# Kernel tuning notes

Measured on AMD Instinct MI355X. Metric: run time of the kernel, lower is better.

Reference implementation:

```python
import jax, jax.numpy as jnp
import numpy as np

# Static problem constants (must match setup_inputs)
NUM_GRAPHS = 64      # batch_size = int(batch[-1]) + 1
PTS_PER_GRAPH = 512
RATIO = 16           # centroids per graph
HEADS = 4
IN_CH = 64           # = out_channels per head (concat=False -> mean over heads)
NEG_SLOPE = 0.2


def setup_inputs() -> dict:
    key = jax.random.key(0)
    ks = jax.random.split(key, 8)
    N = NUM_GRAPHS * PTS_PER_GRAPH
    x = jax.random.normal(ks[0], (N, IN_CH), dtype=jnp.float32)
    edge_index = jnp.zeros((2, 2), dtype=jnp.int64)  # unused by forward
    batch = (jnp.arange(N) // PTS_PER_GRAPH).astype(jnp.int64)
    xcent_base = jax.random.normal(ks[1], (RATIO, IN_CH), dtype=jnp.float32)
    W_l = jax.random.normal(ks[2], (IN_CH, HEADS * IN_CH), dtype=jnp.float32) / np.sqrt(IN_CH)
    b_l = jax.random.normal(ks[3], (HEADS * IN_CH,), dtype=jnp.float32) * 0.01
    W_r = jax.random.normal(ks[4], (IN_CH, HEADS * IN_CH), dtype=jnp.float32) / np.sqrt(IN_CH)
    b_r = jax.random.normal(ks[5], (HEADS * IN_CH,), dtype=jnp.float32) * 0.01
    att = jax.random.normal(ks[6], (HEADS, IN_CH), dtype=jnp.float32) / np.sqrt(IN_CH)
    bias = jax.random.normal(ks[7], (IN_CH,), dtype=jnp.float32) * 0.01
    return {"x": x, "edge_index": edge_index, "batch": batch,
            "xcent_base": xcent_base, "W_l": W_l, "b_l": b_l,
            "W_r": W_r, "b_r": b_r, "att": att, "bias": bias}


def _bipart_pool(x, batch, xcent_base, W_l, b_l, W_r, b_r, att, bias):
    N = x.shape[0]
    B = NUM_GRAPHS
    Nc = B * RATIO  # number of centroid (target) nodes

    # Dense bipartite edges: each source node -> all RATIO centroids of its graph.
    src = jnp.repeat(jnp.arange(N, dtype=jnp.int32), RATIO)                     # [E]
    dst = jnp.tile(jnp.arange(RATIO, dtype=jnp.int32), N) \
        + jnp.repeat(batch.astype(jnp.int32), RATIO) * RATIO                    # [E]

    # PyG GATv2Conv(add_self_loops=True): remove src==dst edges, then add
    # self loops (i,i) for i < min(N_src, N_dst) = Nc. Keep static shapes by
    # masking the removed edges instead of deleting them.
    self_idx = jnp.arange(Nc, dtype=jnp.int32)
    src_f = jnp.concatenate([src, self_idx])
    dst_f = jnp.concatenate([dst, self_idx])
    drop = jnp.concatenate([src == dst, jnp.zeros((Nc,), dtype=bool)])          # [E+Nc]

    # Linear projections (source and target sides)
    x_l = (x @ W_l + b_l).reshape(N, HEADS, IN_CH)                              # [N,H,C]
    xcent = jnp.tile(xcent_base, (B, 1))                                        # [Nc,IN]
    x_r = (xcent @ W_r + b_r).reshape(Nc, HEADS, IN_CH)                         # [Nc,H,C]

    # GATv2 attention: leaky_relu(x_i + x_j) . att, softmax per target node
    xj = x_l[src_f]                                                             # [E',H,C]
    g = jax.nn.leaky_relu(xj + x_r[dst_f], NEG_SLOPE)
    alpha = jnp.einsum('ehc,hc->eh', g, att)                                    # [E',H]
    alpha = jnp.where(drop[:, None], jnp.float32(-1e30), alpha)
    amax = jax.ops.segment_max(alpha, dst_f, num_segments=Nc)                   # [Nc,H]
    e = jnp.exp(alpha - amax[dst_f])
    den = jax.ops.segment_sum(e, dst_f, num_segments=Nc)                        # [Nc,H]
    w = e / den[dst_f]                                                          # [E',H]

    out = jax.ops.segment_sum(w[..., None] * xj, dst_f, num_segments=Nc)        # [Nc,H,C]
    out = out.mean(axis=1) + bias                                               # concat=False -> mean heads
    return out.reshape(B, RATIO, IN_CH)


def reference(x, edge_index, batch, xcent_base, W_l, b_l, W_r, b_r, att, bias):
    xcent = _bipart_pool(x, batch, xcent_base, W_l, b_l, W_r, b_r, att, bias)
    batchcent = jnp.repeat(jnp.arange(NUM_GRAPHS, dtype=jnp.int64), RATIO)
    return xcent, batchcent
```

## Files before the change

### kernel.cpp

```cpp
#include <hip/hip_runtime.h>

#define PTS 512
#define CH  64

using s8v = __attribute__((ext_vector_type(8))) short;
using f4v = __attribute__((ext_vector_type(4))) float;

static __device__ __forceinline__ unsigned short f2b(float f) {
    unsigned u = __float_as_uint(f);
    return (unsigned short)((u + 0x7FFFu + ((u >> 16) & 1u)) >> 16);
}
static __device__ __forceinline__ float b2f(unsigned short s) {
    return __uint_as_float((unsigned)s << 16);
}

__global__ __launch_bounds__(256) void k0(
    const float* __restrict__ xcb, const float* __restrict__ W_r,
    const float* __restrict__ b_r, const float* __restrict__ att,
    const float* __restrict__ bias,
    float* __restrict__ xr_ws, float* __restrict__ sxr_ws,
    float* __restrict__ out)
{
    __shared__ float s_row[256];
    const int blk = blockIdx.x, tid = threadIdx.x;
    if (blk < 16) {
        const int h = blk >> 2, rq = blk & 3;
        const int rl = tid >> 6, c = tid & 63;
        const int r = rq * 4 + rl;
        float acc = b_r[h * 64 + c];
        for (int k = 0; k < 64; ++k)
            acc = fmaf(xcb[r * 64 + k], W_r[k * 256 + h * 64 + c], acc);
        xr_ws[(h * 16 + r) * 64 + c] = acc;
        s_row[rl * 64 + c] = acc;
        __syncthreads();
        if (tid < 4) {
            float s = 0.f;
            for (int cc = 0; cc < 64; ++cc)
                s = fmaf(s_row[tid * 64 + cc], att[h * 64 + cc], s);
            sxr_ws[h * 16 + rq * 4 + tid] = s;
        }
    } else if (blk < 32) {
        const int base = (blk - 16) * 4096;
        float4 bv = *(const float4*)(bias + ((tid * 4) & 63));
#pragma unroll
        for (int j = 0; j < 4; ++j)
            *(float4*)(out + base + j * 1024 + tid * 4) = bv;
    } else {
        const int c = tid * 4;
        *(float4*)(out + 65536 + c) = make_float4(
            (float)(c >> 4), (float)((c + 1) >> 4),
            (float)((c + 2) >> 4), (float)((c + 3) >> 4));
    }
}

__global__ __launch_bounds__(512, 1) void kmain(
    const float* __restrict__ x, const float* __restrict__ W_l,
    const float* __restrict__ b_l, const float* __restrict__ att,
    const float* __restrict__ xr_ws, const float* __restrict__ sxr_ws,
    float* __restrict__ out)
{
    __shared__ __align__(16) float s_buf[16384];
    __shared__ __align__(16) float s_e[8192];
    __shared__ __align__(16) unsigned short s_wt[4096];
    __shared__ __align__(16) float s_xls[1024];
    __shared__ __align__(16) float s_y[1024];
    __shared__ float s_dpart[128];
    __shared__ float s_es[16], s_dns[16], s_inv[16];

    unsigned short* s_xl   = (unsigned short*)s_buf;
    float*          s_part = s_buf;

    const int tid = threadIdx.x;
    const int h = blockIdx.x >> 6;
    const int b = blockIdx.x & 63;
    const int lane = tid & 63;
    const int w = __builtin_amdgcn_readfirstlane(tid >> 6);

    {
        const int c = tid >> 3, kk0 = (tid & 7) * 8;
        s8v wv;
#pragma unroll
        for (int j = 0; j < 8; ++j)
            wv[j] = (short)f2b(W_l[(kk0 + j) * 256 + h * 64 + c]);
        *(s8v*)&s_wt[c * 64 + (kk0 ^ ((c & 7) << 3))] = wv;
    }
    __syncthreads();

    {
        const int r0 = w * 2;
        const float* xg0 = x + (size_t)(b * 16 + r0) * 64;
        const float* xg1 = xg0 + 64;
        float a0 = b_l[h * 64 + lane], a1 = a0;
#pragma unroll
        for (int j8 = 0; j8 < 8; ++j8) {
            s8v wraw = *(const s8v*)&s_wt[lane * 64 + ((j8 * 8) ^ ((lane & 7) << 3))];
#pragma unroll
            for (int j = 0; j < 8; ++j) {
                const float wvf = b2f((unsigned short)wraw[j]);
                a0 = fmaf(xg0[j8 * 8 + j], wvf, a0);
                a1 = fmaf(xg1[j8 * 8 + j], wvf, a1);
            }
        }
        s_xls[r0 * 64 + lane] = a0;
        s_xls[(r0 + 1) * 64 + lane] = a1;

        const float at = att[h * 64 + lane];
        float sx0 = at * a0, ab0 = at * fabsf(a0 + xr_ws[(h * 16 + r0) * 64 + lane]);
        float sx1 = at * a1, ab1 = at * fabsf(a1 + xr_ws[(h * 16 + r0 + 1) * 64 + lane]);
#pragma unroll
        for (int off = 32; off >= 1; off >>= 1) {
            sx0 += __shfl_xor(sx0, off); ab0 += __shfl_xor(ab0, off);
            sx1 += __shfl_xor(sx1, off); ab1 += __shfl_xor(ab1, off);
        }
        if (lane == 0) {
            s_es[r0]     = __expf(0.6f * (sx0 + sxr_ws[h * 16 + r0])     + 0.4f * ab0);
            s_es[r0 + 1] = __expf(0.6f * (sx1 + sxr_ws[h * 16 + r0 + 1]) + 0.4f * ab1);
        }
    }

    {
        const int l15 = lane & 15, quad = lane >> 4;
        const size_t row0 = (size_t)b * PTS + w * 64;
        f4v acc[4][4];
        const f4v zf = {0.f, 0.f, 0.f, 0.f};
#pragma unroll
        for (int m = 0; m < 4; ++m)
#pragma unroll
            for (int n = 0; n < 4; ++n) acc[m][n] = zf;

#pragma unroll
        for (int ks = 0; ks < 2; ++ks) {
            s8v Af[4], Bf[4];
#pragma unroll
            for (int m = 0; m < 4; ++m) {
                const float* xp = x + (row0 + m * 16 + l15) * 64 + ks * 32 + quad * 8;
                float4 u0 = *(const float4*)xp;
                float4 u1 = *(const float4*)(xp + 4);
                s8v a;
                a[0] = (short)f2b(u0.x); a[1] = (short)f2b(u0.y);
                a[2] = (short)f2b(u0.z); a[3] = (short)f2b(u0.w);
                a[4] = (short)f2b(u1.x); a[5] = (short)f2b(u1.y);
                a[6] = (short)f2b(u1.z); a[7] = (short)f2b(u1.w);
                Af[m] = a;
            }
#pragma unroll
            for (int n = 0; n < 4; ++n) {
                const int cc = n * 16 + l15;
                Bf[n] = *(const s8v*)&s_wt[cc * 64 +
                        ((ks * 32 + quad * 8) ^ ((cc & 7) << 3))];
            }
#pragma unroll
            for (int m = 0; m < 4; ++m)
#pragma unroll
                for (int n = 0; n < 4; ++n)
                    acc[m][n] = __builtin_amdgcn_mfma_f32_16x16x32_bf16(
                        Af[m], Bf[n], acc[m][n], 0, 0, 0);
        }

        float blv[4];
#pragma unroll
        for (int n = 0; n < 4; ++n) blv[n] = b_l[h * 64 + n * 16 + l15];
#pragma unroll
        for (int m = 0; m < 4; ++m)
#pragma unroll
            for (int n = 0; n < 4; ++n) {
                const int cc = n * 16 + l15;
#pragma unroll
                for (int qq = 0; qq < 4; ++qq) {
                    const int row = w * 64 + m * 16 + quad * 4 + qq;
                    s_xl[row * 64 + (cc ^ ((row & 7) << 3))] =
                        f2b(acc[m][n][qq] + blv[n]);
                }
            }
    }
    __syncthreads();

    {
        const int i = tid, sw = i & 3, xsw = (i & 7) << 3;
        const float* attw = att + h * 64;
        const float* xrw  = xr_ws + h * 1024;
        float ac[16];
#pragma unroll
        for (int r = 0; r < 16; ++r) ac[r] = 0.f;
        float sxl = 0.f;

#pragma unroll
        for (int half = 0; half < 2; ++half) {
            const int cb = half * 32;
            float xlv[32], atv[32];
#pragma unroll
            for (int c8 = 0; c8 < 4; ++c8) {
                const int ch0 = cb + c8 * 8;
                uint4 raw = *(const uint4*)&s_xl[i * 64 + (ch0 ^ xsw)];
                unsigned uu[4] = {raw.x, raw.y, raw.z, raw.w};
#pragma unroll
                for (int p = 0; p < 4; ++p) {
                    xlv[c8 * 8 + 2 * p]     = __uint_as_float(uu[p] << 16);
                    xlv[c8 * 8 + 2 * p + 1] = __uint_as_float(uu[p] & 0xffff0000u);
                }
            }
#pragma unroll
            for (int cq = 0; cq < 8; ++cq) {
                float4 a4 = *(const float4*)(attw + cb + cq * 4);
                atv[cq * 4 + 0] = a4.x; atv[cq * 4 + 1] = a4.y;
                atv[cq * 4 + 2] = a4.z; atv[cq * 4 + 3] = a4.w;
            }
#pragma unroll
            for (int t = 0; t < 32; ++t) sxl = fmaf(atv[t], xlv[t], sxl);

#pragma unroll 2
            for (int r = 0; r < 16; ++r) {
                const float4* xrp = (const float4*)(xrw + r * 64 + cb);
                float a = 0.f;
#pragma unroll
                for (int cq = 0; cq < 8; ++cq) {
                    float4 x4 = xrp[cq];
                    a = fmaf(atv[cq * 4 + 0], fabsf(xlv[cq * 4 + 0] + x4.x), a);
                    a = fmaf(atv[cq * 4 + 1], fabsf(xlv[cq * 4 + 1] + x4.y), a);
                    a = fmaf(atv[cq * 4 + 2], fabsf(xlv[cq * 4 + 2] + x4.z), a);
                    a = fmaf(atv[cq * 4 + 3], fabsf(xlv[cq * 4 + 3] + x4.w), a);
                }
                ac[r] += a;
            }
        }
        float ev[16];
#pragma unroll
        for (int r = 0; r < 16; ++r) {
            float a = 0.6f * (sxl + sxr_ws[h * 16 + r]) + 0.4f * ac[r];
            float e = __expf(a);
            if (b == 0 && i == r) e = 0.f;
            ev[r] = e;
        }
        float4* se4 = (float4*)s_e;
#pragma unroll
        for (int q = 0; q < 4; ++q)
            se4[i * 4 + (q ^ sw)] = make_float4(ev[q * 4 + 0], ev[q * 4 + 1],
                                                ev[q * 4 + 2], ev[q * 4 + 3]);
#pragma unroll
        for (int r = 0; r < 16; ++r) {
            float s = ev[r];
#pragma unroll
            for (int off = 32; off >= 1; off >>= 1) s += __shfl_xor(s, off);
            if (lane == 0) s_dpart[w * 16 + r] = s;
        }
    }
    __syncthreads();

    if (tid < 16) {
        float dns = 0.f;
#pragma unroll
        for (int ww = 0; ww < 8; ++ww) dns += s_dpart[ww * 16 + tid];
        const float es = s_es[tid];
        s_dns[tid] = dns;
        s_inv[tid] = 1.f / (dns + es);
    }

    {
        const int kt = tid & 15, rt = (tid >> 4) & 3, is = tid >> 6;
        float y4[4][4];
#pragma unroll
        for (int i = 0; i < 4; ++i)
#pragma unroll
            for (int j = 0; j < 4; ++j) y4[i][j] = 0.f;

        const float* xb = x + ((size_t)b * PTS + is * 64) * 64;
        const float4* se4 = (const float4*)s_e;
        for (int ii0 = 0; ii0 < 64; ii0 += 8) {
            float4 xv[8], evv[8];
#pragma unroll
            for (int u = 0; u < 8; ++u)
                xv[u] = *(const float4*)(xb + (ii0 + u) * 64 + kt * 4);
#pragma unroll
            for (int u = 0; u < 8; ++u) {
                const int i = is * 64 + ii0 + u;
                evv[u] = se4[i * 4 + (rt ^ (i & 3))];
            }
#pragma unroll
            for (int u = 0; u < 8; ++u) {
                const float4 xvu = xv[u], ev = evv[u];
                y4[0][0] = fmaf(ev.x, xvu.x, y4[0][0]); y4[0][1] = fmaf(ev.x, xvu.y, y4[0][1]);
                y4[0][2] = fmaf(ev.x, xvu.z, y4[0][2]); y4[0][3] = fmaf(ev.x, xvu.w, y4[0][3]);
                y4[1][0] = fmaf(ev.y, xvu.x, y4[1][0]); y4[1][1] = fmaf(ev.y, xvu.y, y4[1][1]);
                y4[1][2] = fmaf(ev.y, xvu.z, y4[1][2]); y4[1][3] = fmaf(ev.y, xvu.w, y4[1][3]);
                y4[2][0] = fmaf(ev.z, xvu.x, y4[2][0]); y4[2][1] = fmaf(ev.z, xvu.y, y4[2][1]);
                y4[2][2] = fmaf(ev.z, xvu.z, y4[2][2]); y4[2][3] = fmaf(ev.z, xvu.w, y4[2][3]);
                y4[3][0] = fmaf(ev.w, xvu.x, y4[3][0]); y4[3][1] = fmaf(ev.w, xvu.y, y4[3][1]);
                y4[3][2] = fmaf(ev.w, xvu.z, y4[3][2]); y4[3][3] = fmaf(ev.w, xvu.w, y4[3][3]);
            }
        }
#pragma unroll
        for (int rr = 0; rr < 4; ++rr)
            *(float4*)&s_part[is * 1024 + (rt * 4 + rr) * 64 + kt * 4] =
                make_float4(y4[rr][0], y4[rr][1], y4[rr][2], y4[rr][3]);
    }
    __syncthreads();

    for (int o = tid; o < 1024; o += 512) {
        float s = 0.f;
#pragma unroll
        for (int sl = 0; sl < 8; ++sl) s += s_part[sl * 1024 + o];
        s_y[o] = s;
    }
    __syncthreads();

    for (int o = tid; o < 1024; o += 512) {
        const int r = o >> 6, ch = o & 63;
        float a = 0.f;
        const float* yr = s_y + r * 64;
#pragma unroll
        for (int k = 0; k < 64; ++k)
            a = fmaf(yr[k], W_l[k * 256 + h * 64 + ch], a);
        float val = (a + s_dns[r] * b_l[h * 64 + ch]
                     + s_es[r] * s_xls[r * 64 + ch]) * s_inv[r];
        atomicAdd(&out[(b * 16 + r) * 64 + ch], 0.25f * val);
    }
}

extern "C" void kernel_launch(void* const* d_in, const int* in_sizes, int n_in,
                              void* d_out, int out_size, void* d_ws, size_t ws_size,
                              hipStream_t stream) {
    (void)in_sizes; (void)n_in; (void)out_size; (void)ws_size;
    const float* x    = (const float*)d_in[0];
    const float* xcb  = (const float*)d_in[3];
    const float* W_l  = (const float*)d_in[4];
    const float* b_l  = (const float*)d_in[5];
    const float* W_r  = (const float*)d_in[6];
    const float* b_r  = (const float*)d_in[7];
    const float* att  = (const float*)d_in[8];
    const float* bias = (const float*)d_in[9];
    float* out = (float*)d_out;

    float* wsf = (float*)d_ws;
    float* xr_ws  = wsf;
    float* sxr_ws = wsf + 4096;

    hipLaunchKernelGGL(k0, dim3(33), dim3(256), 0, stream,
                       xcb, W_r, b_r, att, bias, xr_ws, sxr_ws, out);
    hipLaunchKernelGGL(kmain, dim3(256), dim3(512), 0, stream,
                       x, W_l, b_l, att, xr_ws, sxr_ws, out);
}
```

Baseline: 111.5 us.

## Split per-graph-head work into halves and add a finalize kernel replacing atomics

```diff
diff --git a/kernel.cpp b/kernel.cpp
--- a/kernel.cpp
+++ b/kernel.cpp
@@ -17,110 +17,68 @@
 __global__ __launch_bounds__(256) void k0(
     const float* __restrict__ xcb, const float* __restrict__ W_r,
     const float* __restrict__ b_r, const float* __restrict__ att,
-    const float* __restrict__ bias,
-    float* __restrict__ xr_ws, float* __restrict__ sxr_ws,
-    float* __restrict__ out)
+    float* __restrict__ xr_ws, float* __restrict__ sxr_ws)
 {
     __shared__ float s_row[256];
     const int blk = blockIdx.x, tid = threadIdx.x;
-    if (blk < 16) {
-        const int h = blk >> 2, rq = blk & 3;
-        const int rl = tid >> 6, c = tid & 63;
-        const int r = rq * 4 + rl;
-        float acc = b_r[h * 64 + c];
-        for (int k = 0; k < 64; ++k)
-            acc = fmaf(xcb[r * 64 + k], W_r[k * 256 + h * 64 + c], acc);
-        xr_ws[(h * 16 + r) * 64 + c] = acc;
-        s_row[rl * 64 + c] = acc;
-        __syncthreads();
-        if (tid < 4) {
-            float s = 0.f;
-            for (int cc = 0; cc < 64; ++cc)
-                s = fmaf(s_row[tid * 64 + cc], att[h * 64 + cc], s);
-            sxr_ws[h * 16 + rq * 4 + tid] = s;
-        }
-    } else if (blk < 32) {
-        const int base = (blk - 16) * 4096;
-        float4 bv = *(const float4*)(bias + ((tid * 4) & 63));
-#pragma unroll
-        for (int j = 0; j < 4; ++j)
-            *(float4*)(out + base + j * 1024 + tid * 4) = bv;
-    } else {
-        const int c = tid * 4;
-        *(float4*)(out + 65536 + c) = make_float4(
-            (float)(c >> 4), (float)((c + 1) >> 4),
-            (float)((c + 2) >> 4), (float)((c + 3) >> 4));
-    }
-}
-
-__global__ __launch_bounds__(512, 1) void kmain(
+    const int h = blk >> 2, rq = blk & 3;
+    const int rl = tid >> 6, c = tid & 63;
+    const int r = rq * 4 + rl;
+    float acc = b_r[h * 64 + c];
+    for (int k = 0; k < 64; ++k)
+        acc = fmaf(xcb[r * 64 + k], W_r[k * 256 + h * 64 + c], acc);
+    xr_ws[(h * 16 + r) * 64 + c] = acc;
+    s_row[rl * 64 + c] = acc;
+    __syncthreads();
+    if (tid < 4) {
+        float s = 0.f;
+        for (int cc = 0; cc < 64; ++cc)
+            s = fmaf(s_row[tid * 64 + cc], att[h * 64 + cc], s);
+        sxr_ws[h * 16 + rq * 4 + tid] = s;
+    }
+}
+
+__global__ __launch_bounds__(256, 2) void kmain(
     const float* __restrict__ x, const float* __restrict__ W_l,
     const float* __restrict__ b_l, const float* __restrict__ att,
     const float* __restrict__ xr_ws, const float* __restrict__ sxr_ws,
-    float* __restrict__ out)
+    float* __restrict__ y_ws, float* __restrict__ den_ws)
 {
-    __shared__ __align__(16) float s_buf[16384];
-    __shared__ __align__(16) float s_e[8192];
+    __shared__ __align__(16) float s_buf[8192];
+    __shared__ __align__(16) float s_e[4096];
     __shared__ __align__(16) unsigned short s_wt[4096];
-    __shared__ __align__(16) float s_xls[1024];
-    __shared__ __align__(16) float s_y[1024];
-    __shared__ float s_dpart[128];
-    __shared__ float s_es[16], s_dns[16], s_inv[16];
+    __shared__ float s_dpart[64];
 
     unsigned short* s_xl   = (unsigned short*)s_buf;
     float*          s_part = s_buf;
 
     const int tid = threadIdx.x;
-    const int h = blockIdx.x >> 6;
-    const int b = blockIdx.x & 63;
+    const int L = blockIdx.x;
+    const int j = L >> 3;
+    const int b = (L & 7) * 8 + (j >> 3);
+    const int h = (j & 7) >> 1;
+    const int half = j & 1;
+    const int bh2 = ((b * 4 + h) << 1) | half;
     const int lane = tid & 63;
     const int w = __builtin_amdgcn_readfirstlane(tid >> 6);
 
     {
-        const int c = tid >> 3, kk0 = (tid & 7) * 8;
-        s8v wv;
-#pragma unroll
-        for (int j = 0; j < 8; ++j)
-            wv[j] = (short)f2b(W_l[(kk0 + j) * 256 + h * 64 + c]);
-        *(s8v*)&s_wt[c * 64 + (kk0 ^ ((c & 7) << 3))] = wv;
-    }
-    __syncthreads();
-
-    {
-        const int r0 = w * 2;
-        const float* xg0 = x + (size_t)(b * 16 + r0) * 64;
-        const float* xg1 = xg0 + 64;
-        float a0 = b_l[h * 64 + lane], a1 = a0;
-#pragma unroll
-        for (int j8 = 0; j8 < 8; ++j8) {
-            s8v wraw = *(const s8v*)&s_wt[lane * 64 + ((j8 * 8) ^ ((lane & 7) << 3))];
-#pragma unroll
-            for (int j = 0; j < 8; ++j) {
-                const float wvf = b2f((unsigned short)wraw[j]);
-                a0 = fmaf(xg0[j8 * 8 + j], wvf, a0);
-                a1 = fmaf(xg1[j8 * 8 + j], wvf, a1);
-            }
-        }
-        s_xls[r0 * 64 + lane] = a0;
-        s_xls[(r0 + 1) * 64 + lane] = a1;
-
-        const float at = att[h * 64 + lane];
-        float sx0 = at * a0, ab0 = at * fabsf(a0 + xr_ws[(h * 16 + r0) * 64 + lane]);
-        float sx1 = at * a1, ab1 = at * fabsf(a1 + xr_ws[(h * 16 + r0 + 1) * 64 + lane]);
-#pragma unroll
-        for (int off = 32; off >= 1; off >>= 1) {
-            sx0 += __shfl_xor(sx0, off); ab0 += __shfl_xor(ab0, off);
-            sx1 += __shfl_xor(sx1, off); ab1 += __shfl_xor(ab1, off);
-        }
-        if (lane == 0) {
-            s_es[r0]     = __expf(0.6f * (sx0 + sxr_ws[h * 16 + r0])     + 0.4f * ab0);
-            s_es[r0 + 1] = __expf(0.6f * (sx1 + sxr_ws[h * 16 + r0 + 1]) + 0.4f * ab1);
-        }
-    }
+        const int c = tid >> 2, kq = tid & 3;
+#pragma unroll
+        for (int j8 = 0; j8 < 2; ++j8) {
+            const int kk = kq * 16 + j8 * 8;
+            s8v wv;
+#pragma unroll
+            for (int t = 0; t < 8; ++t)
+                wv[t] = (short)f2b(W_l[(kk + t) * 256 + h * 64 + c]);
+            *(s8v*)&s_wt[c * 64 + (kk ^ ((c & 7) << 3))] = wv;
+        }
+    }
+    __syncthreads();
 
     {
         const int l15 = lane & 15, quad = lane >> 4;
-        const size_t row0 = (size_t)b * PTS + w * 64;
+        const size_t row0 = (size_t)b * PTS + half * 256 + w * 64;
         f4v acc[4][4];
         const f4v zf = {0.f, 0.f, 0.f, 0.f};
 #pragma unroll
@@ -185,8 +143,8 @@
         float sxl = 0.f;
 
 #pragma unroll
-        for (int half = 0; half < 2; ++half) {
-            const int cb = half * 32;
+        for (int hf = 0; hf < 2; ++hf) {
+            const int cb = hf * 32;
             float xlv[32], atv[32];
 #pragma unroll
             for (int c8 = 0; c8 < 4; ++c8) {
@@ -228,7 +186,7 @@
         for (int r = 0; r < 16; ++r) {
             float a = 0.6f * (sxl + sxr_ws[h * 16 + r]) + 0.4f * ac[r];
             float e = __expf(a);
-            if (b == 0 && i == r) e = 0.f;
+            if (b == 0 && half == 0 && i == r) e = 0.f;
             ev[r] = e;
         }
         float4* se4 = (float4*)s_e;
@@ -247,12 +205,10 @@
     __syncthreads();
 
     if (tid < 16) {
-        float dns = 0.f;
-#pragma unroll
-        for (int ww = 0; ww < 8; ++ww) dns += s_dpart[ww * 16 + tid];
-        const float es = s_es[tid];
-        s_dns[tid] = dns;
-        s_inv[tid] = 1.f / (dns + es);
+        float d = 0.f;
+#pragma unroll
+        for (int ww = 0; ww < 4; ++ww) d += s_dpart[ww * 16 + tid];
+        den_ws[bh2 * 16 + tid] = d;
     }
 
     {
@@ -261,9 +217,9 @@
 #pragma unroll
         for (int i = 0; i < 4; ++i)
 #pragma unroll
-            for (int j = 0; j < 4; ++j) y4[i][j] = 0.f;
-
-        const float* xb = x + ((size_t)b * PTS + is * 64) * 64;
+            for (int jj = 0; jj < 4; ++jj) y4[i][jj] = 0.f;
+
+        const float* xb = x + ((size_t)b * PTS + half * 256 + is * 64) * 64;
         const float4* se4 = (const float4*)s_e;
         for (int ii0 = 0; ii0 < 64; ii0 += 8) {
             float4 xv[8], evv[8];
@@ -295,25 +251,96 @@
     }
     __syncthreads();
 
-    for (int o = tid; o < 1024; o += 512) {
+    for (int o = tid; o < 1024; o += 256) {
         float s = 0.f;
 #pragma unroll
-        for (int sl = 0; sl < 8; ++sl) s += s_part[sl * 1024 + o];
-        s_y[o] = s;
-    }
-    __syncthreads();
-
-    for (int o = tid; o < 1024; o += 512) {
-        const int r = o >> 6, ch = o & 63;
-        float a = 0.f;
-        const float* yr = s_y + r * 64;
-#pragma unroll
+        for (int sl = 0; sl < 4; ++sl) s += s_part[sl * 1024 + o];
+        y_ws[bh2 * 1024 + o] = s;
+    }
+}
+
+__global__ __launch_bounds__(256) void kfin(
+    const float* __restrict__ x, const float* __restrict__ W_l,
+    const float* __restrict__ b_l, const float* __restrict__ att,
+    const float* __restrict__ xr_ws, const float* __restrict__ sxr_ws,
+    const float* __restrict__ bias,
+    const float* __restrict__ y_ws, const float* __restrict__ den_ws,
+    float* __restrict__ out)
+{
+    __shared__ __align__(16) float s_yt[1024];
+    __shared__ __align__(16) float s_xls[1024];
+    __shared__ float s_dent[16], s_es[16];
+
+    const int tid = threadIdx.x;
+    const int b = blockIdx.x >> 2, rg = blockIdx.x & 3;
+
+#pragma unroll
+    for (int jj = 0; jj < 4; ++jj) {
+        const int flat = tid + jj * 256;
+        const int hh = flat >> 8, rl = (flat >> 6) & 3, k = flat & 63;
+        const size_t base = (size_t)((b * 4 + hh) * 2) * 1024 + (rg * 4 + rl) * 64 + k;
+        s_yt[flat] = y_ws[base] + y_ws[base + 1024];
+    }
+    if (tid < 16) {
+        const int hh = tid >> 2, rl = tid & 3;
+        const int base = ((b * 4 + hh) * 2) * 16 + rg * 4 + rl;
+        s_dent[tid] = den_ws[base] + den_ws[base + 16];
+    }
+#pragma unroll
+    for (int jj = 0; jj < 4; ++jj) {
+        const int flat = tid + jj * 256;
+        const int hh = flat >> 8, rl = (flat >> 6) & 3, c = flat & 63;
+        const int r = rg * 4 + rl;
+        float acc = b_l[hh * 64 + c];
         for (int k = 0; k < 64; ++k)
-            a = fmaf(yr[k], W_l[k * 256 + h * 64 + ch], a);
-        float val = (a + s_dns[r] * b_l[h * 64 + ch]
-                     + s_es[r] * s_xls[r * 64 + ch]) * s_inv[r];
-        atomicAdd(&out[(b * 16 + r) * 64 + ch], 0.25f * val);
-    }
+            acc = fmaf(x[(size_t)(b * 16 + r) * 64 + k],
+                       W_l[k * 256 + hh * 64 + c], acc);
+        s_xls[flat] = acc;
+    }
+    __syncthreads();
+
+    {
+        const int g = tid >> 4, l16 = tid & 15;
+        const int hh = g >> 2, rl = g & 3, r = rg * 4 + rl;
+        float sx = 0.f, ab = 0.f;
+#pragma unroll
+        for (int q = 0; q < 4; ++q) {
+            const int cc = l16 * 4 + q;
+            const float a = att[hh * 64 + cc];
+            const float xv = s_xls[(g << 6) + cc];
+            sx = fmaf(a, xv, sx);
+            ab = fmaf(a, fabsf(xv + xr_ws[(hh * 16 + r) * 64 + cc]), ab);
+        }
+#pragma unroll
+        for (int off = 8; off >= 1; off >>= 1) {
+            sx += __shfl_xor(sx, off);
+            ab += __shfl_xor(ab, off);
+        }
+        if (l16 == 0)
+            s_es[g] = __expf(0.6f * (sx + sxr_ws[hh * 16 + r]) + 0.4f * ab);
+    }
+    __syncthreads();
+
+    {
+        const int rl = tid >> 6, c = tid & 63;
+        const int r = rg * 4 + rl;
+        float num = 0.f;
+#pragma unroll
+        for (int hh = 0; hh < 4; ++hh) {
+            float t = 0.f;
+            const float* yr = s_yt + hh * 256 + rl * 64;
+#pragma unroll
+            for (int k = 0; k < 64; ++k)
+                t = fmaf(yr[k], W_l[k * 256 + hh * 64 + c], t);
+            const float es = s_es[hh * 4 + rl];
+            const float dt = s_dent[hh * 4 + rl];
+            num += (t + dt * b_l[hh * 64 + c] + es * s_xls[hh * 256 + rl * 64 + c])
+                   / (dt + es);
+        }
+        out[(size_t)(b * 16 + r) * 64 + c] = bias[c] + 0.25f * num;
+    }
+    if (rg == 0 && tid < 16)
+        out[65536 + b * 16 + tid] = (float)b;
 }
 
 extern "C" void kernel_launch(void* const* d_in, const int* in_sizes, int n_in,
@@ -333,9 +360,13 @@
     float* wsf = (float*)d_ws;
     float* xr_ws  = wsf;
     float* sxr_ws = wsf + 4096;
-
-    hipLaunchKernelGGL(k0, dim3(33), dim3(256), 0, stream,
-                       xcb, W_r, b_r, att, bias, xr_ws, sxr_ws, out);
-    hipLaunchKernelGGL(kmain, dim3(256), dim3(512), 0, stream,
-                       x, W_l, b_l, att, xr_ws, sxr_ws, out);
-}
+    float* y_ws   = wsf + 4224;
+    float* den_ws = wsf + 528512;
+
+    hipLaunchKernelGGL(k0, dim3(16), dim3(256), 0, stream,
+                       xcb, W_r, b_r, att, xr_ws, sxr_ws);
+    hipLaunchKernelGGL(kmain, dim3(512), dim3(256), 0, stream,
+                       x, W_l, b_l, att, xr_ws, sxr_ws, y_ws, den_ws);
+    hipLaunchKernelGGL(kfin, dim3(256), dim3(256), 0, stream,
+                       x, W_l, b_l, att, xr_ws, sxr_ws, bias, y_ws, den_ws, out);
+}
```

After: 123.6 us. 1.11x slower.

## Split each graph-head block into two point halves and reduce in a finalize kernel

Applied to the files above, without the earlier changes.

```diff
diff --git a/kernel.cpp b/kernel.cpp
--- a/kernel.cpp
+++ b/kernel.cpp
@@ -17,62 +17,49 @@
 __global__ __launch_bounds__(256) void k0(
     const float* __restrict__ xcb, const float* __restrict__ W_r,
     const float* __restrict__ b_r, const float* __restrict__ att,
-    const float* __restrict__ bias,
-    float* __restrict__ xr_ws, float* __restrict__ sxr_ws,
-    float* __restrict__ out)
+    float* __restrict__ xr_ws, float* __restrict__ sxr_ws)
 {
     __shared__ float s_row[256];
     const int blk = blockIdx.x, tid = threadIdx.x;
-    if (blk < 16) {
-        const int h = blk >> 2, rq = blk & 3;
-        const int rl = tid >> 6, c = tid & 63;
-        const int r = rq * 4 + rl;
-        float acc = b_r[h * 64 + c];
-        for (int k = 0; k < 64; ++k)
-            acc = fmaf(xcb[r * 64 + k], W_r[k * 256 + h * 64 + c], acc);
-        xr_ws[(h * 16 + r) * 64 + c] = acc;
-        s_row[rl * 64 + c] = acc;
-        __syncthreads();
-        if (tid < 4) {
-            float s = 0.f;
-            for (int cc = 0; cc < 64; ++cc)
-                s = fmaf(s_row[tid * 64 + cc], att[h * 64 + cc], s);
-            sxr_ws[h * 16 + rq * 4 + tid] = s;
-        }
-    } else if (blk < 32) {
-        const int base = (blk - 16) * 4096;
-        float4 bv = *(const float4*)(bias + ((tid * 4) & 63));
-#pragma unroll
-        for (int j = 0; j < 4; ++j)
-            *(float4*)(out + base + j * 1024 + tid * 4) = bv;
-    } else {
-        const int c = tid * 4;
-        *(float4*)(out + 65536 + c) = make_float4(
-            (float)(c >> 4), (float)((c + 1) >> 4),
-            (float)((c + 2) >> 4), (float)((c + 3) >> 4));
-    }
-}
-
-__global__ __launch_bounds__(512, 1) void kmain(
+    const int h = blk >> 2, rq = blk & 3;
+    const int rl = tid >> 6, c = tid & 63;
+    const int r = rq * 4 + rl;
+    float acc = b_r[h * 64 + c];
+    for (int k = 0; k < 64; ++k)
+        acc = fmaf(xcb[r * 64 + k], W_r[k * 256 + h * 64 + c], acc);
+    xr_ws[(h * 16 + r) * 64 + c] = acc;
+    s_row[rl * 64 + c] = acc;
+    __syncthreads();
+    if (tid < 4) {
+        float s = 0.f;
+        for (int cc = 0; cc < 64; ++cc)
+            s = fmaf(s_row[tid * 64 + cc], att[h * 64 + cc], s);
+        sxr_ws[h * 16 + rq * 4 + tid] = s;
+    }
+}
+
+__global__ __launch_bounds__(512, 4) void kmain(
     const float* __restrict__ x, const float* __restrict__ W_l,
     const float* __restrict__ b_l, const float* __restrict__ att,
     const float* __restrict__ xr_ws, const float* __restrict__ sxr_ws,
-    float* __restrict__ out)
+    float* __restrict__ num_ws, float* __restrict__ den_ws,
+    float* __restrict__ xls_ws, float* __restrict__ es_ws)
 {
-    __shared__ __align__(16) float s_buf[16384];
-    __shared__ __align__(16) float s_e[8192];
+    __shared__ __align__(16) float s_buf[8192];
+    __shared__ __align__(16) float s_e[4096];
     __shared__ __align__(16) unsigned short s_wt[4096];
-    __shared__ __align__(16) float s_xls[1024];
-    __shared__ __align__(16) float s_y[1024];
-    __shared__ float s_dpart[128];
-    __shared__ float s_es[16], s_dns[16], s_inv[16];
+    __shared__ float s_dpart[64];
 
     unsigned short* s_xl   = (unsigned short*)s_buf;
     float*          s_part = s_buf;
+    float*          s_y    = s_e;
 
     const int tid = threadIdx.x;
-    const int h = blockIdx.x >> 6;
-    const int b = blockIdx.x & 63;
+    const int b    = blockIdx.x >> 3;
+    const int h    = (blockIdx.x >> 1) & 3;
+    const int half = blockIdx.x & 1;
+    const int bh   = b * 4 + h;
+    const int bh2  = bh * 2 + half;
     const int lane = tid & 63;
     const int w = __builtin_amdgcn_readfirstlane(tid >> 6);
 
@@ -86,7 +73,7 @@
     }
     __syncthreads();
 
-    {
+    if (half == 0) {
         const int r0 = w * 2;
         const float* xg0 = x + (size_t)(b * 16 + r0) * 64;
         const float* xg1 = xg0 + 64;
@@ -101,8 +88,8 @@
                 a1 = fmaf(xg1[j8 * 8 + j], wvf, a1);
             }
         }
-        s_xls[r0 * 64 + lane] = a0;
-        s_xls[(r0 + 1) * 64 + lane] = a1;
+        xls_ws[bh * 1024 + r0 * 64 + lane]       = a0;
+        xls_ws[bh * 1024 + (r0 + 1) * 64 + lane] = a1;
 
         const float at = att[h * 64 + lane];
         float sx0 = at * a0, ab0 = at * fabsf(a0 + xr_ws[(h * 16 + r0) * 64 + lane]);
@@ -113,26 +100,28 @@
             sx1 += __shfl_xor(sx1, off); ab1 += __shfl_xor(ab1, off);
         }
         if (lane == 0) {
-            s_es[r0]     = __expf(0.6f * (sx0 + sxr_ws[h * 16 + r0])     + 0.4f * ab0);
-            s_es[r0 + 1] = __expf(0.6f * (sx1 + sxr_ws[h * 16 + r0 + 1]) + 0.4f * ab1);
+            es_ws[bh * 16 + r0] =
+                __expf(0.6f * (sx0 + sxr_ws[h * 16 + r0])     + 0.4f * ab0);
+            es_ws[bh * 16 + r0 + 1] =
+                __expf(0.6f * (sx1 + sxr_ws[h * 16 + r0 + 1]) + 0.4f * ab1);
         }
     }
 
     {
         const int l15 = lane & 15, quad = lane >> 4;
-        const size_t row0 = (size_t)b * PTS + w * 64;
-        f4v acc[4][4];
+        const size_t row0 = (size_t)b * PTS + half * 256 + w * 32;
+        f4v acc[2][4];
         const f4v zf = {0.f, 0.f, 0.f, 0.f};
 #pragma unroll
-        for (int m = 0; m < 4; ++m)
+        for (int m = 0; m < 2; ++m)
 #pragma unroll
             for (int n = 0; n < 4; ++n) acc[m][n] = zf;
 
 #pragma unroll
         for (int ks = 0; ks < 2; ++ks) {
-            s8v Af[4], Bf[4];
-#pragma unroll
-            for (int m = 0; m < 4; ++m) {
+            s8v Af[2], Bf[4];
+#pragma unroll
+            for (int m = 0; m < 2; ++m) {
                 const float* xp = x + (row0 + m * 16 + l15) * 64 + ks * 32 + quad * 8;
                 float4 u0 = *(const float4*)xp;
                 float4 u1 = *(const float4*)(xp + 4);
@@ -150,7 +139,7 @@
                         ((ks * 32 + quad * 8) ^ ((cc & 7) << 3))];
             }
 #pragma unroll
-            for (int m = 0; m < 4; ++m)
+            for (int m = 0; m < 2; ++m)
 #pragma unroll
                 for (int n = 0; n < 4; ++n)
                     acc[m][n] = __builtin_amdgcn_mfma_f32_16x16x32_bf16(
@@ -161,13 +150,13 @@
 #pragma unroll
         for (int n = 0; n < 4; ++n) blv[n] = b_l[h * 64 + n * 16 + l15];
 #pragma unroll
-        for (int m = 0; m < 4; ++m)
+        for (int m = 0; m < 2; ++m)
 #pragma unroll
             for (int n = 0; n < 4; ++n) {
                 const int cc = n * 16 + l15;
 #pragma unroll
                 for (int qq = 0; qq < 4; ++qq) {
-                    const int row = w * 64 + m * 16 + quad * 4 + qq;
+                    const int row = w * 32 + m * 16 + quad * 4 + qq;
                     s_xl[row * 64 + (cc ^ ((row & 7) << 3))] =
                         f2b(acc[m][n][qq] + blv[n]);
                 }
@@ -176,17 +165,18 @@
     __syncthreads();
 
     {
-        const int i = tid, sw = i & 3, xsw = (i & 7) << 3;
+        const int i = tid & 255, rh = tid >> 8, rbase = rh * 8;
+        const int sw = i & 3, xsw = (i & 7) << 3;
         const float* attw = att + h * 64;
         const float* xrw  = xr_ws + h * 1024;
-        float ac[16];
-#pragma unroll
-        for (int r = 0; r < 16; ++r) ac[r] = 0.f;
+        float ac[8];
+#pragma unroll
+        for (int r = 0; r < 8; ++r) ac[r] = 0.f;
         float sxl = 0.f;
 
 #pragma unroll
-        for (int half = 0; half < 2; ++half) {
-            const int cb = half * 32;
+        for (int hf = 0; hf < 2; ++hf) {
+            const int cb = hf * 32;
             float xlv[32], atv[32];
 #pragma unroll
             for (int c8 = 0; c8 < 4; ++c8) {
@@ -209,8 +199,8 @@
             for (int t = 0; t < 32; ++t) sxl = fmaf(atv[t], xlv[t], sxl);
 
 #pragma unroll 2
-            for (int r = 0; r < 16; ++r) {
-                const float4* xrp = (const float4*)(xrw + r * 64 + cb);
+            for (int rr = 0; rr < 8; ++rr) {
+                const float4* xrp = (const float4*)(xrw + (rbase + rr) * 64 + cb);
                 float a = 0.f;
 #pragma unroll
                 for (int cq = 0; cq < 8; ++cq) {
@@ -220,39 +210,38 @@
                     a = fmaf(atv[cq * 4 + 2], fabsf(xlv[cq * 4 + 2] + x4.z), a);
                     a = fmaf(atv[cq * 4 + 3], fabsf(xlv[cq * 4 + 3] + x4.w), a);
                 }
-                ac[r] += a;
-            }
-        }
-        float ev[16];
-#pragma unroll
-        for (int r = 0; r < 16; ++r) {
-            float a = 0.6f * (sxl + sxr_ws[h * 16 + r]) + 0.4f * ac[r];
+                ac[rr] += a;
+            }
+        }
+        float ev[8];
+#pragma unroll
+        for (int rr = 0; rr < 8; ++rr) {
+            const int r = rbase + rr;
+            float a = 0.6f * (sxl + sxr_ws[h * 16 + r]) + 0.4f * ac[rr];
             float e = __expf(a);
-            if (b == 0 && i == r) e = 0.f;
-            ev[r] = e;
+            if (b == 0 && half == 0 && i == r) e = 0.f;
+            ev[rr] = e;
         }
         float4* se4 = (float4*)s_e;
-#pragma unroll
-        for (int q = 0; q < 4; ++q)
-            se4[i * 4 + (q ^ sw)] = make_float4(ev[q * 4 + 0], ev[q * 4 + 1],
-                                                ev[q * 4 + 2], ev[q * 4 + 3]);
-#pragma unroll
-        for (int r = 0; r < 16; ++r) {
-            float s = ev[r];
+        se4[i * 4 + ((2 * rh)     ^ sw)] = make_float4(ev[0], ev[1], ev[2], ev[3]);
+        se4[i * 4 + ((2 * rh + 1) ^ sw)] = make_float4(ev[4], ev[5], ev[6], ev[7]);
+#pragma unroll
+        for (int rr = 0; rr < 8; ++rr) {
+            float s = ev[rr];
 #pragma unroll
             for (int off = 32; off >= 1; off >>= 1) s += __shfl_xor(s, off);
-            if (lane == 0) s_dpart[w * 16 + r] = s;
+            if (lane == 0) s_dpart[w * 8 + rr] = s;
         }
     }
     __syncthreads();
 
     if (tid < 16) {
-        float dns = 0.f;
-#pragma unroll
-        for (int ww = 0; ww < 8; ++ww) dns += s_dpart[ww * 16 + tid];
-        const float es = s_es[tid];
-        s_dns[tid] = dns;
-        s_inv[tid] = 1.f / (dns + es);
+        const int rh = tid >> 3;
+        float d = 0.f;
+#pragma unroll
+        for (int ww = 0; ww < 4; ++ww)
+            d += s_dpart[(rh * 4 + ww) * 8 + (tid & 7)];
+        den_ws[bh2 * 16 + tid] = d;
     }
 
     {
@@ -261,18 +250,18 @@
 #pragma unroll
         for (int i = 0; i < 4; ++i)
 #pragma unroll
-            for (int j = 0; j < 4; ++j) y4[i][j] = 0.f;
-
-        const float* xb = x + ((size_t)b * PTS + is * 64) * 64;
+            for (int jj = 0; jj < 4; ++jj) y4[i][jj] = 0.f;
+
+        const float* xb = x + ((size_t)b * PTS + half * 256 + is * 32) * 64;
         const float4* se4 = (const float4*)s_e;
-        for (int ii0 = 0; ii0 < 64; ii0 += 8) {
+        for (int ii0 = 0; ii0 < 32; ii0 += 8) {
             float4 xv[8], evv[8];
 #pragma unroll
             for (int u = 0; u < 8; ++u)
                 xv[u] = *(const float4*)(xb + (ii0 + u) * 64 + kt * 4);
 #pragma unroll
             for (int u = 0; u < 8; ++u) {
-                const int i = is * 64 + ii0 + u;
+                const int i = is * 32 + ii0 + u;
                 evv[u] = se4[i * 4 + (rt ^ (i & 3))];
             }
 #pragma unroll
@@ -310,10 +299,36 @@
 #pragma unroll
         for (int k = 0; k < 64; ++k)
             a = fmaf(yr[k], W_l[k * 256 + h * 64 + ch], a);
-        float val = (a + s_dns[r] * b_l[h * 64 + ch]
-                     + s_es[r] * s_xls[r * 64 + ch]) * s_inv[r];
-        atomicAdd(&out[(b * 16 + r) * 64 + ch], 0.25f * val);
-    }
+        num_ws[bh2 * 1024 + o] = a;
+    }
+}
+
+__global__ __launch_bounds__(256) void kfin(
+    const float* __restrict__ b_l, const float* __restrict__ bias,
+    const float* __restrict__ num_ws, const float* __restrict__ den_ws,
+    const float* __restrict__ xls_ws, const float* __restrict__ es_ws,
+    float* __restrict__ out)
+{
+    const int tid = threadIdx.x;
+    const int b = blockIdx.x >> 2, rg = blockIdx.x & 3;
+    const int rl = tid >> 6, c = tid & 63;
+    const int r = rg * 4 + rl;
+
+    float val = 0.f;
+#pragma unroll
+    for (int hh = 0; hh < 4; ++hh) {
+        const int bh = b * 4 + hh;
+        const float n0 = num_ws[(size_t)(bh * 2)     * 1024 + r * 64 + c];
+        const float n1 = num_ws[(size_t)(bh * 2 + 1) * 1024 + r * 64 + c];
+        const float dt = den_ws[(bh * 2) * 16 + r] + den_ws[(bh * 2 + 1) * 16 + r];
+        const float es = es_ws[bh * 16 + r];
+        const float xls = xls_ws[(size_t)bh * 1024 + r * 64 + c];
+        val += (n0 + n1 + dt * b_l[hh * 64 + c] + es * xls) / (dt + es);
+    }
+    out[(size_t)(b * 16 + r) * 64 + c] = bias[c] + 0.25f * val;
+
+    if (rg == 0 && tid < 16)
+        out[65536 + b * 16 + tid] = (float)b;
 }
 
 extern "C" void kernel_launch(void* const* d_in, const int* in_sizes, int n_in,
@@ -333,9 +348,16 @@
     float* wsf = (float*)d_ws;
     float* xr_ws  = wsf;
     float* sxr_ws = wsf + 4096;
-
-    hipLaunchKernelGGL(k0, dim3(33), dim3(256), 0, stream,
-                       xcb, W_r, b_r, att, bias, xr_ws, sxr_ws, out);
-    hipLaunchKernelGGL(kmain, dim3(256), dim3(512), 0, stream,
-                       x, W_l, b_l, att, xr_ws, sxr_ws, out);
-}
+    float* num_ws = wsf + 4224;
+    float* den_ws = wsf + 528512;
+    float* xls_ws = wsf + 536704;
+    float* es_ws  = wsf + 798848;
+
+    hipLaunchKernelGGL(k0, dim3(16), dim3(256), 0, stream,
+                       xcb, W_r, b_r, att, xr_ws, sxr_ws);
+    hipLaunchKernelGGL(kmain, dim3(512), dim3(512), 0, stream,
+                       x, W_l, b_l, att, xr_ws, sxr_ws,
+                       num_ws, den_ws, xls_ws, es_ws);
+    hipLaunchKernelGGL(kfin, dim3(256), dim3(256), 0, stream,
+                       b_l, bias, num_ws, den_ws, xls_ws, es_ws, out);
+}
```

After: 139.7 us. 25.3% more time.

## Double kmain block to 1024 threads and halve per-thread row work

Applied to the files above, without the earlier changes.

```diff
diff --git a/kernel.cpp b/kernel.cpp
--- a/kernel.cpp
+++ b/kernel.cpp
@@ -53,7 +53,7 @@
     }
 }
 
-__global__ __launch_bounds__(512, 1) void kmain(
+__global__ __launch_bounds__(1024, 4) void kmain(
     const float* __restrict__ x, const float* __restrict__ W_l,
     const float* __restrict__ b_l, const float* __restrict__ att,
     const float* __restrict__ xr_ws, const float* __restrict__ sxr_ws,
@@ -76,7 +76,7 @@
     const int lane = tid & 63;
     const int w = __builtin_amdgcn_readfirstlane(tid >> 6);
 
-    {
+    if (tid < 512) {
         const int c = tid >> 3, kk0 = (tid & 7) * 8;
         s8v wv;
 #pragma unroll
@@ -87,52 +87,44 @@
     __syncthreads();
 
     {
-        const int r0 = w * 2;
-        const float* xg0 = x + (size_t)(b * 16 + r0) * 64;
-        const float* xg1 = xg0 + 64;
-        float a0 = b_l[h * 64 + lane], a1 = a0;
+        const float* xg = x + (size_t)(b * 16 + w) * 64;
+        float a0 = b_l[h * 64 + lane];
 #pragma unroll
         for (int j8 = 0; j8 < 8; ++j8) {
             s8v wraw = *(const s8v*)&s_wt[lane * 64 + ((j8 * 8) ^ ((lane & 7) << 3))];
 #pragma unroll
-            for (int j = 0; j < 8; ++j) {
-                const float wvf = b2f((unsigned short)wraw[j]);
-                a0 = fmaf(xg0[j8 * 8 + j], wvf, a0);
-                a1 = fmaf(xg1[j8 * 8 + j], wvf, a1);
-            }
-        }
-        s_xls[r0 * 64 + lane] = a0;
-        s_xls[(r0 + 1) * 64 + lane] = a1;
+            for (int j = 0; j < 8; ++j)
+                a0 = fmaf(xg[j8 * 8 + j], b2f((unsigned short)wraw[j]), a0);
+        }
+        s_xls[w * 64 + lane] = a0;
 
         const float at = att[h * 64 + lane];
-        float sx0 = at * a0, ab0 = at * fabsf(a0 + xr_ws[(h * 16 + r0) * 64 + lane]);
-        float sx1 = at * a1, ab1 = at * fabsf(a1 + xr_ws[(h * 16 + r0 + 1) * 64 + lane]);
+        float sx = at * a0;
+        float ab = at * fabsf(a0 + xr_ws[(h * 16 + w) * 64 + lane]);
 #pragma unroll
         for (int off = 32; off >= 1; off >>= 1) {
-            sx0 += __shfl_xor(sx0, off); ab0 += __shfl_xor(ab0, off);
-            sx1 += __shfl_xor(sx1, off); ab1 += __shfl_xor(ab1, off);
-        }
-        if (lane == 0) {
-            s_es[r0]     = __expf(0.6f * (sx0 + sxr_ws[h * 16 + r0])     + 0.4f * ab0);
-            s_es[r0 + 1] = __expf(0.6f * (sx1 + sxr_ws[h * 16 + r0 + 1]) + 0.4f * ab1);
-        }
+            sx += __shfl_xor(sx, off);
+            ab += __shfl_xor(ab, off);
+        }
+        if (lane == 0)
+            s_es[w] = __expf(0.6f * (sx + sxr_ws[h * 16 + w]) + 0.4f * ab);
     }
 
     {
         const int l15 = lane & 15, quad = lane >> 4;
-        const size_t row0 = (size_t)b * PTS + w * 64;
-        f4v acc[4][4];
+        const size_t row0 = (size_t)b * PTS + w * 32;
+        f4v acc[2][4];
         const f4v zf = {0.f, 0.f, 0.f, 0.f};
 #pragma unroll
-        for (int m = 0; m < 4; ++m)
+        for (int m = 0; m < 2; ++m)
 #pragma unroll
             for (int n = 0; n < 4; ++n) acc[m][n] = zf;
 
 #pragma unroll
         for (int ks = 0; ks < 2; ++ks) {
-            s8v Af[4], Bf[4];
-#pragma unroll
-            for (int m = 0; m < 4; ++m) {
+            s8v Af[2], Bf[4];
+#pragma unroll
+            for (int m = 0; m < 2; ++m) {
                 const float* xp = x + (row0 + m * 16 + l15) * 64 + ks * 32 + quad * 8;
                 float4 u0 = *(const float4*)xp;
                 float4 u1 = *(const float4*)(xp + 4);
@@ -150,7 +142,7 @@
                         ((ks * 32 + quad * 8) ^ ((cc & 7) << 3))];
             }
 #pragma unroll
-            for (int m = 0; m < 4; ++m)
+            for (int m = 0; m < 2; ++m)
 #pragma unroll
                 for (int n = 0; n < 4; ++n)
                     acc[m][n] = __builtin_amdgcn_mfma_f32_16x16x32_bf16(
@@ -161,13 +153,13 @@
 #pragma unroll
         for (int n = 0; n < 4; ++n) blv[n] = b_l[h * 64 + n * 16 + l15];
 #pragma unroll
-        for (int m = 0; m < 4; ++m)
+        for (int m = 0; m < 2; ++m)
 #pragma unroll
             for (int n = 0; n < 4; ++n) {
                 const int cc = n * 16 + l15;
 #pragma unroll
                 for (int qq = 0; qq < 4; ++qq) {
-                    const int row = w * 64 + m * 16 + quad * 4 + qq;
+                    const int row = w * 32 + m * 16 + quad * 4 + qq;
                     s_xl[row * 64 + (cc ^ ((row & 7) << 3))] =
                         f2b(acc[m][n][qq] + blv[n]);
                 }
@@ -176,17 +168,18 @@
     __syncthreads();
 
     {
-        const int i = tid, sw = i & 3, xsw = (i & 7) << 3;
+        const int i = tid & 511, rh = tid >> 9, rbase = rh * 8;
+        const int sw = i & 3, xsw = (i & 7) << 3;
         const float* attw = att + h * 64;
         const float* xrw  = xr_ws + h * 1024;
-        float ac[16];
-#pragma unroll
-        for (int r = 0; r < 16; ++r) ac[r] = 0.f;
+        float ac[8];
+#pragma unroll
+        for (int r = 0; r < 8; ++r) ac[r] = 0.f;
         float sxl = 0.f;
 
 #pragma unroll
-        for (int half = 0; half < 2; ++half) {
-            const int cb = half * 32;
+        for (int hf = 0; hf < 2; ++hf) {
+            const int cb = hf * 32;
             float xlv[32], atv[32];
 #pragma unroll
             for (int c8 = 0; c8 < 4; ++c8) {
@@ -209,8 +202,8 @@
             for (int t = 0; t < 32; ++t) sxl = fmaf(atv[t], xlv[t], sxl);
 
 #pragma unroll 2
-            for (int r = 0; r < 16; ++r) {
-                const float4* xrp = (const float4*)(xrw + r * 64 + cb);
+            for (int rr = 0; rr < 8; ++rr) {
+                const float4* xrp = (const float4*)(xrw + (rbase + rr) * 64 + cb);
                 float a = 0.f;
 #pragma unroll
                 for (int cq = 0; cq < 8; ++cq) {
@@ -220,36 +213,37 @@
                     a = fmaf(atv[cq * 4 + 2], fabsf(xlv[cq * 4 + 2] + x4.z), a);
                     a = fmaf(atv[cq * 4 + 3], fabsf(xlv[cq * 4 + 3] + x4.w), a);
                 }
-                ac[r] += a;
-            }
-        }
-        float ev[16];
-#pragma unroll
-        for (int r = 0; r < 16; ++r) {
-            float a = 0.6f * (sxl + sxr_ws[h * 16 + r]) + 0.4f * ac[r];
+                ac[rr] += a;
+            }
+        }
+        float ev[8];
+#pragma unroll
+        for (int rr = 0; rr < 8; ++rr) {
+            const int r = rbase + rr;
+            float a = 0.6f * (sxl + sxr_ws[h * 16 + r]) + 0.4f * ac[rr];
             float e = __expf(a);
             if (b == 0 && i == r) e = 0.f;
-            ev[r] = e;
+            ev[rr] = e;
         }
         float4* se4 = (float4*)s_e;
-#pragma unroll
-        for (int q = 0; q < 4; ++q)
-            se4[i * 4 + (q ^ sw)] = make_float4(ev[q * 4 + 0], ev[q * 4 + 1],
-                                                ev[q * 4 + 2], ev[q * 4 + 3]);
-#pragma unroll
-        for (int r = 0; r < 16; ++r) {
-            float s = ev[r];
+        se4[i * 4 + ((2 * rh)     ^ sw)] = make_float4(ev[0], ev[1], ev[2], ev[3]);
+        se4[i * 4 + ((2 * rh + 1) ^ sw)] = make_float4(ev[4], ev[5], ev[6], ev[7]);
+#pragma unroll
+        for (int rr = 0; rr < 8; ++rr) {
+            float s = ev[rr];
 #pragma unroll
             for (int off = 32; off >= 1; off >>= 1) s += __shfl_xor(s, off);
-            if (lane == 0) s_dpart[w * 16 + r] = s;
+            if (lane == 0) s_dpart[w * 8 + rr] = s;
         }
     }
     __syncthreads();
 
     if (tid < 16) {
+        const int wb = (tid >> 3) * 8;
         float dns = 0.f;
 #pragma unroll
-        for (int ww = 0; ww < 8; ++ww) dns += s_dpart[ww * 16 + tid];
+        for (int j = 0; j < 8; ++j)
+            dns += s_dpart[(wb + j) * 8 + (tid & 7)];
         const float es = s_es[tid];
         s_dns[tid] = dns;
         s_inv[tid] = 1.f / (dns + es);
@@ -261,18 +255,18 @@
 #pragma unroll
         for (int i = 0; i < 4; ++i)
 #pragma unroll
-            for (int j = 0; j < 4; ++j) y4[i][j] = 0.f;
-
-        const float* xb = x + ((size_t)b * PTS + is * 64) * 64;
+            for (int jj = 0; jj < 4; ++jj) y4[i][jj] = 0.f;
+
+        const float* xb = x + ((size_t)b * PTS + is * 32) * 64;
         const float4* se4 = (const float4*)s_e;
-        for (int ii0 = 0; ii0 < 64; ii0 += 8) {
+        for (int ii0 = 0; ii0 < 32; ii0 += 8) {
             float4 xv[8], evv[8];
 #pragma unroll
             for (int u = 0; u < 8; ++u)
                 xv[u] = *(const float4*)(xb + (ii0 + u) * 64 + kt * 4);
 #pragma unroll
             for (int u = 0; u < 8; ++u) {
-                const int i = is * 64 + ii0 + u;
+                const int i = is * 32 + ii0 + u;
                 evv[u] = se4[i * 4 + (rt ^ (i & 3))];
             }
 #pragma unroll
@@ -295,16 +289,16 @@
     }
     __syncthreads();
 
-    for (int o = tid; o < 1024; o += 512) {
+    {
         float s = 0.f;
 #pragma unroll
-        for (int sl = 0; sl < 8; ++sl) s += s_part[sl * 1024 + o];
-        s_y[o] = s;
-    }
-    __syncthreads();
-
-    for (int o = tid; o < 1024; o += 512) {
-        const int r = o >> 6, ch = o & 63;
+        for (int sl = 0; sl < 16; ++sl) s += s_part[sl * 1024 + tid];
+        s_y[tid] = s;
+    }
+    __syncthreads();
+
+    {
+        const int r = tid >> 6, ch = tid & 63;
         float a = 0.f;
         const float* yr = s_y + r * 64;
 #pragma unroll
@@ -336,6 +330,6 @@
 
     hipLaunchKernelGGL(k0, dim3(33), dim3(256), 0, stream,
                        xcb, W_r, b_r, att, bias, xr_ws, sxr_ws, out);
-    hipLaunchKernelGGL(kmain, dim3(256), dim3(512), 0, stream,
+    hipLaunchKernelGGL(kmain, dim3(256), dim3(1024), 0, stream,
                        x, W_l, b_l, att, xr_ws, sxr_ws, out);
 }
```

After: 351.0 us. 3.15x slower.
